# Performance work log

Measured on AMD Instinct MI355X. Metric: run time of the kernel, lower is better.

The kernel has to match this reference:

```python
import jax, jax.numpy as jnp
import numpy as np
import math

KV_STRIDE = 2
Q_STRIDE = 1
WAVE_LEN = 1000.0
POS_MAG = 1.0


def _pos_embed(h, w, h_kv, w_kv, q_stride, kv_stride, feat_dim):
    # Sinusoidal relative-position embeddings, matching get_position_embedding.
    h_idx = jnp.arange(h, dtype=jnp.float32) * q_stride
    w_idx = jnp.arange(w, dtype=jnp.float32) * q_stride
    h_kv_idx = jnp.arange(h_kv, dtype=jnp.float32) * kv_stride
    w_kv_idx = jnp.arange(w_kv, dtype=jnp.float32) * kv_stride
    h_diff = (h_idx[:, None] - h_kv_idx[None, :]) * POS_MAG  # (h, h_kv)
    w_diff = (w_idx[:, None] - w_kv_idx[None, :]) * POS_MAG  # (w, w_kv)
    feat_range = jnp.arange(feat_dim // 4, dtype=jnp.float32)
    dim_mat = WAVE_LEN ** (4.0 / feat_dim * feat_range)  # (feat_dim//4,)
    wd = w_diff[:, :, None] / dim_mat  # (w, w_kv, F)
    hd = h_diff[:, :, None] / dim_mat  # (h, h_kv, F)
    emb_x = jnp.concatenate([jnp.sin(wd), jnp.cos(wd)], axis=2)  # (w, w_kv, feat_dim//2)
    emb_y = jnp.concatenate([jnp.sin(hd), jnp.cos(hd)], axis=2)  # (h, h_kv, feat_dim//2)
    return emb_x, emb_y


def setup_inputs() -> dict:
    key = jax.random.key(0)
    ks = jax.random.split(key, 11)
    C = 288
    s = 1.0 / math.sqrt(C)
    return {
        'x_input': jax.random.normal(ks[0], (2, C, 64, 64), jnp.float32),
        'Wq': jax.random.normal(ks[1], (C, C), jnp.float32) * s,
        'Wk': jax.random.normal(ks[2], (C, C), jnp.float32) * s,
        'Wv': jax.random.normal(ks[3], (C, C), jnp.float32) * s,
        'Wx': jax.random.normal(ks[4], (C, C // 2), jnp.float32) * s,
        'Wy': jax.random.normal(ks[5], (C, C // 2), jnp.float32) * s,
        'Wproj': jax.random.normal(ks[6], (C, C), jnp.float32) * s,
        'bproj': jax.random.normal(ks[7], (C,), jnp.float32) * 0.02,
        'Wc': jax.random.normal(ks[8], (9, C), jnp.float32) * s,
        'bc': jax.random.normal(ks[9], (9,), jnp.float32) * 0.02,
        'gamma': jax.random.normal(ks[10], (1,), jnp.float32),
    }


def reference(x_input, Wq, Wk, Wv, Wx, Wy, Wproj, bproj, Wc, bc, gamma):
    M = Wc.shape[0]                       # num_mixtures
    n, C, h, w = x_input.shape
    d = Wq.shape[0] // M                  # qk_embed_dim (== v_dim)
    x_q = x_input                         # q_stride == 1
    x_kv = x_input[:, :, ::KV_STRIDE, ::KV_STRIDE]  # AvgPool2d(k=1, stride=2)
    h_kv, w_kv = x_kv.shape[2], x_kv.shape[3]

    # 1x1 convs as channel GEMMs
    q = jnp.einsum('nchw,oc->nohw', x_q, Wq).reshape(n, M, d, h * w)
    q = q.transpose(0, 1, 3, 2)                                    # (n,M,hw,d)
    k = jnp.einsum('nchw,oc->nohw', x_kv, Wk).reshape(n, M, d, h_kv * w_kv)

    emb_x, emb_y = _pos_embed(h, w, h_kv, w_kv, Q_STRIDE, KV_STRIDE, C)
    inv_sqrt2 = 1.0 / math.sqrt(2.0)
    pf_x = (emb_x @ Wx.T).reshape(w, w_kv, M, d).transpose(2, 0, 1, 3) * inv_sqrt2  # (M,w,w_kv,d)
    pf_y = (emb_y @ Wy.T).reshape(h, h_kv, M, d).transpose(2, 0, 1, 3) * inv_sqrt2  # (M,h,h_kv,d)

    energy = jnp.matmul(q, k).reshape(n, M, h, w, h_kv, w_kv)
    q5 = q.reshape(n, M, h, w, d)
    e_x = jnp.einsum('nmhwd,mwvd->nmhwv', q5, pf_x)  # (n,M,h,w,w_kv)
    e_y = jnp.einsum('nmhwd,mhud->nmhwu', q5, pf_y)  # (n,M,h,w,h_kv)
    energy = energy + e_x[:, :, :, :, None, :] + e_y[:, :, :, :, :, None]
    energy = energy.reshape(n, M, h * w, h_kv * w_kv)
    attn = jax.nn.softmax(energy, axis=3)

    # Learned per-mixture gating from mean query context
    context = q.transpose(0, 1, 3, 2).reshape(n, M * d, h * w).mean(axis=2)  # (n, M*d)
    mix_w = jax.nn.softmax(context @ Wc.T + bc, axis=1)                      # (n, M)
    attn = jnp.sum(attn * mix_w[:, :, None, None], axis=1)                   # (n,hw,hw_kv)

    v = jnp.einsum('nchw,oc->nohw', x_kv, Wv).reshape(n, M * d, h_kv * w_kv)
    v = v.transpose(0, 2, 1)                                                 # (n,hw_kv,M*d)
    out = jnp.matmul(attn, v).transpose(0, 2, 1).reshape(n, M * d, h, w)
    out = jnp.einsum('nchw,oc->nohw', out, Wproj) + bproj[None, :, None, None]
    return gamma[0] * out + x_input
```

## Files before the change

kernel.cpp:

```cpp
#include <hip/hip_runtime.h>
#include <math.h>

#define NB     2
#define CDIM   288
#define HW     4096
#define PKV    1024
#define MHEAD  9
#define DHEAD  32

typedef __attribute__((ext_vector_type(8))) short bf16x8;
typedef __attribute__((ext_vector_type(4))) float f32x4;

__device__ inline unsigned short f2bf(float x) {
    unsigned int u = __float_as_uint(x);
    u = (u + 0x7fffu + ((u >> 16) & 1u)) >> 16;
    return (unsigned short)u;
}


__global__ __launch_bounds__(256) void prep(const float* __restrict__ X,
        const float* __restrict__ Wq, const float* __restrict__ Wk,
        const float* __restrict__ Wv, const float* __restrict__ Wproj,
        const float* __restrict__ Wx, const float* __restrict__ Wy,
        unsigned short* __restrict__ XF, unsigned short* __restrict__ WFq,
        unsigned short* __restrict__ WFk, unsigned short* __restrict__ WFv,
        unsigned short* __restrict__ WFp, float* __restrict__ WTx,
        float* __restrict__ WTy, float* __restrict__ MX) {
    __shared__ float t32[32][133];
    __shared__ float t16[16][17];
    __shared__ float red[4];
    int b = blockIdx.x;
    int tid = threadIdx.x;
    if (b < 576) {
        int bx = b % 32, by = (b / 32) % 9, n = b / 288;
        int j0 = bx * 128, c0 = by * 32;
        int c = tid >> 3, f = tid & 7;
        const float* src = &X[((size_t)n * CDIM + c0 + c) * HW + j0];
#pragma unroll
        for (int l = 0; l < 4; ++l) {
            float4 v = *(const float4*)&src[(f + l * 8) * 4];
            *(float4*)&t32[c][(f + l * 8) * 4] = v;
        }
        __syncthreads();
        int cc = c0 >> 5;
#pragma unroll
        for (int l = 0; l < 4; ++l) {
            int g = l * 256 + tid;
            int s = g >> 7;
            int w = g & 127;
            int lane = w >> 1, e0 = (w & 1) * 4;
            int jl = s * 16 + (lane & 15);
            int cb = (lane >> 4) * 8 + e0;
            unsigned int w0 = f2bf(t32[cb + 0][jl]) | ((unsigned int)f2bf(t32[cb + 1][jl]) << 16);
            unsigned int w1 = f2bf(t32[cb + 2][jl]) | ((unsigned int)f2bf(t32[cb + 3][jl]) << 16);
            int jt = (j0 >> 4) + s;
            unsigned short* O = XF + (size_t)n * HW * CDIM + ((size_t)jt * 9 + cc) * 512 + lane * 8 + e0;
            uint2 pk = { w0, w1 };
            *(uint2*)O = pk;
        }
    } else if (b < 900) {
        int u = b - 576;
        int bx = u % 9, by = (u / 9) % 18, bz = u / 162;
        const float* W = bz ? Wy : Wx;
        float* WT      = bz ? WTy : WTx;
        int f0 = bx * 16, o0 = by * 16;
        int tx = tid & 15, ty = tid >> 4;
        t16[ty][tx] = W[(o0 + ty) * 144 + f0 + tx];
        __syncthreads();
        WT[(f0 + ty) * 288 + o0 + tx] = t16[tx][ty];
    } else if (b < 1062) {
        int t = b - 900;
        int sub = tid >> 6, lane = tid & 63;
        int ot = t / 9, cc = t % 9;
        const float* W = (sub == 0) ? Wq : (sub == 1) ? Wk : (sub == 2) ? Wv : Wproj;
        unsigned short* O = ((sub == 0) ? WFq : (sub == 1) ? WFk : (sub == 2) ? WFv : WFp)
                            + (size_t)t * 512;
        int o  = ot * 16 + (lane & 15);
        int c0 = cc * 32 + (lane >> 4) * 8;
        const float* src = W + (size_t)o * CDIM + c0;
        float4 f0 = *(const float4*)src, f1 = *(const float4*)(src + 4);
        unsigned int v0 = f2bf(f0.x) | ((unsigned int)f2bf(f0.y) << 16);
        unsigned int v1 = f2bf(f0.z) | ((unsigned int)f2bf(f0.w) << 16);
        unsigned int v2 = f2bf(f1.x) | ((unsigned int)f2bf(f1.y) << 16);
        unsigned int v3 = f2bf(f1.z) | ((unsigned int)f2bf(f1.w) << 16);
        uint4 pk = { v0, v1, v2, v3 };
        *(uint4*)(O + lane * 8) = pk;
    } else {
        int bid = b - 1062;
        const float* xr = X + (size_t)bid * HW;
        float s = 0.f;
        for (int j = tid; j < HW; j += 256) s += xr[j];
        for (int off = 32; off > 0; off >>= 1) s += __shfl_xor(s, off, 64);
        if ((tid & 63) == 0) red[tid >> 6] = s;
        __syncthreads();
        if (tid == 0) MX[bid] = (red[0] + red[1] + red[2] + red[3]) * (1.f / 4096.f);
    }
}

__global__ __launch_bounds__(256) void mid(
        const float* __restrict__ WTx, const float* __restrict__ WTy,
        unsigned short* __restrict__ FXb, unsigned short* __restrict__ FYb,
        const float* __restrict__ Wq, const float* __restrict__ MX,
        const float* __restrict__ Wc, const float* __restrict__ bc,
        float* __restrict__ MIXW,
        const unsigned short* __restrict__ WFq, const unsigned short* __restrict__ WFk,
        const unsigned short* __restrict__ WFv, const unsigned short* __restrict__ XF,
        unsigned short* __restrict__ Qf, unsigned short* __restrict__ KF,
        unsigned short* __restrict__ VF) {
    __shared__ float emb[144];
    __shared__ float ctx_s[NB * CDIM];
    __shared__ float lg[18];
    __shared__ __attribute__((aligned(16))) unsigned short tr[4][32][40];
    int b = blockIdx.x;
    int tid = threadIdx.x;

    if (b < 252) {
        int axis = b / 126;
        int dif  = b % 126;
        float diff = (float)(dif - 62);
        if (tid < 72) {
            float dm = expf(6.9077552789821368f * ((float)tid * (1.f / 72.f)));
            float t  = diff / dm;
            emb[tid]      = sinf(t);
            emb[72 + tid] = cosf(t);
        }
        __syncthreads();
        const float* WT = axis ? WTy : WTx;
        unsigned short* F = axis ? FYb : FXb;
        for (int o = tid; o < CDIM; o += 256) {
            float s = 0.f;
#pragma unroll 8
            for (int f = 0; f < 144; ++f) s += emb[f] * WT[f * 288 + o];
            int m = o >> 5, d = o & 31;
            F[(size_t)(m * 8 + (dif >> 4)) * 512 + ((dif & 15) + 16 * (d >> 3)) * 8 + (d & 7)]
                = f2bf(s * 0.70710678118654752f);
        }
    } else if (b == 252) {
        for (int idx = tid; idx < 1152; idx += 256) {
            int d = idx & 31, rr = (idx >> 5) & 1, mm = (idx >> 6) % 9, ax = idx / 576;
            int dif = 126 + rr;
            unsigned short* F = ax ? FYb : FXb;
            F[(size_t)(mm * 8 + 7) * 512 + ((dif & 15) + 16 * (d >> 3)) * 8 + (d & 7)] = 0;
        }
        for (int p = tid; p < NB * CDIM; p += 256) {
            int n = p / CDIM, o = p % CDIM;
            const float* wr = Wq + (size_t)o * CDIM;
            const float* mx = MX + n * CDIM;
            float s = 0.f;
            for (int c = 0; c < CDIM; c += 4) {
                float4 w4 = *(const float4*)&wr[c];
                float4 m4 = *(const float4*)&mx[c];
                s += w4.x * m4.x + w4.y * m4.y + w4.z * m4.z + w4.w * m4.w;
            }
            ctx_s[p] = s;
        }
        __syncthreads();
        if (tid < 18) {
            int n = tid / 9, j = tid % 9;
            float s = bc[j];
            for (int o = 0; o < CDIM; ++o) s += ctx_s[n * CDIM + o] * Wc[j * CDIM + o];
            lg[tid] = s;
        }
        __syncthreads();
        if (tid < 2) {
            float mx = -1e30f;
            for (int j = 0; j < 9; ++j) mx = fmaxf(mx, lg[tid * 9 + j]);
            float e[9], sm = 0.f;
            for (int j = 0; j < 9; ++j) { e[j] = __expf(lg[tid * 9 + j] - mx); sm += e[j]; }
            for (int j = 0; j < 9; ++j) MIXW[tid * 9 + j] = e[j] / sm;
        }
    } else {
        int bx = b - 253;
        int gx = bx % 40;
        int m  = (bx / 40) % 9;
        int n  = bx / 360;
        int wv = tid >> 6, lane = tid & 63;
        int lq = lane & 15, quad = lane >> 4;
        if (gx < 32) {
            int j0 = gx * 128;
            int jw = j0 + wv * 32;
            const unsigned short* Wb = WFq + ((size_t)(m * 2) * 9) * 512 + lane * 8;
            const unsigned short* Xb = XF + (size_t)n * HW * CDIM + ((size_t)(jw >> 4) * 9) * 512 + lane * 8;
            f32x4 acc[2][2] = {};
#pragma unroll
            for (int cc = 0; cc < 9; ++cc) {
                bf16x8 a0 = *(const bf16x8*)(Wb + (size_t)cc * 512);
                bf16x8 a1 = *(const bf16x8*)(Wb + (size_t)(9 + cc) * 512);
                bf16x8 b0 = *(const bf16x8*)(Xb + (size_t)cc * 512);
                bf16x8 b1 = *(const bf16x8*)(Xb + (size_t)(9 + cc) * 512);
                acc[0][0] = __builtin_amdgcn_mfma_f32_16x16x32_bf16(a0, b0, acc[0][0], 0, 0, 0);
                acc[0][1] = __builtin_amdgcn_mfma_f32_16x16x32_bf16(a0, b1, acc[0][1], 0, 0, 0);
                acc[1][0] = __builtin_amdgcn_mfma_f32_16x16x32_bf16(a1, b0, acc[1][0], 0, 0, 0);
                acc[1][1] = __builtin_amdgcn_mfma_f32_16x16x32_bf16(a1, b1, acc[1][1], 0, 0, 0);
            }
#pragma unroll
            for (int oi = 0; oi < 2; ++oi)
#pragma unroll
                for (int ji = 0; ji < 2; ++ji)
#pragma unroll
                    for (int r = 0; r < 4; ++r)
                        tr[wv][ji * 16 + lq][oi * 16 + quad * 4 + r] = f2bf(acc[oi][ji][r]);
            int jl = lane & 31, half = lane >> 5;
            bf16x8 v0 = *(const bf16x8*)&tr[wv][jl][half * 16];
            bf16x8 v1 = *(const bf16x8*)&tr[wv][jl][half * 16 + 8];
            unsigned short* Qm = Qf + ((size_t)(n * MHEAD + m) * HW + jw + jl) * 32 + half * 16;
            *(bf16x8*)Qm = v0;
            *(bf16x8*)(Qm + 8) = v1;
        } else {
            int p0 = (gx - 32) * 128;
            int pw = p0 + wv * 32;
            const unsigned short* XFn = XF + (size_t)n * HW * CDIM;
            size_t bidx[2];
#pragma unroll
            for (int pi = 0; pi < 2; ++pi) {
                int p   = pw + pi * 16 + lq;
                int pos = ((p >> 5) << 7) + ((p & 31) << 1);
                bidx[pi] = ((size_t)(pos >> 4) * 9) * 512 + ((pos & 15) + 16 * quad) * 8;
            }
            const unsigned short* Wkb = WFk + ((size_t)(m * 2) * 9) * 512 + lane * 8;
            const unsigned short* Wvb = WFv + ((size_t)(m * 2) * 9) * 512 + lane * 8;
            f32x4 ak[2][2] = {}, av[2][2] = {};
#pragma unroll
            for (int cc = 0; cc < 9; ++cc) {
                bf16x8 a0k = *(const bf16x8*)(Wkb + (size_t)cc * 512);
                bf16x8 a1k = *(const bf16x8*)(Wkb + (size_t)(9 + cc) * 512);
                bf16x8 a0v = *(const bf16x8*)(Wvb + (size_t)cc * 512);
                bf16x8 a1v = *(const bf16x8*)(Wvb + (size_t)(9 + cc) * 512);
                bf16x8 b0  = *(const bf16x8*)(XFn + bidx[0] + (size_t)cc * 512);
                bf16x8 b1  = *(const bf16x8*)(XFn + bidx[1] + (size_t)cc * 512);
                ak[0][0] = __builtin_amdgcn_mfma_f32_16x16x32_bf16(a0k, b0, ak[0][0], 0, 0, 0);
                ak[0][1] = __builtin_amdgcn_mfma_f32_16x16x32_bf16(a0k, b1, ak[0][1], 0, 0, 0);
                ak[1][0] = __builtin_amdgcn_mfma_f32_16x16x32_bf16(a1k, b0, ak[1][0], 0, 0, 0);
                ak[1][1] = __builtin_amdgcn_mfma_f32_16x16x32_bf16(a1k, b1, ak[1][1], 0, 0, 0);
                av[0][0] = __builtin_amdgcn_mfma_f32_16x16x32_bf16(a0v, b0, av[0][0], 0, 0, 0);
                av[0][1] = __builtin_amdgcn_mfma_f32_16x16x32_bf16(a0v, b1, av[0][1], 0, 0, 0);
                av[1][0] = __builtin_amdgcn_mfma_f32_16x16x32_bf16(a1v, b0, av[1][0], 0, 0, 0);
                av[1][1] = __builtin_amdgcn_mfma_f32_16x16x32_bf16(a1v, b1, av[1][1], 0, 0, 0);
            }
#pragma unroll
            for (int oi = 0; oi < 2; ++oi)
#pragma unroll
                for (int pi = 0; pi < 2; ++pi)
#pragma unroll
                    for (int r = 0; r < 4; ++r)
                        tr[wv][pi * 16 + lq][oi * 16 + quad * 4 + r] = f2bf(ak[oi][pi][r]);
            unsigned short* KFm = KF + (size_t)(n * MHEAD + m) * (PKV * 32);
#pragma unroll
            for (int pi = 0; pi < 2; ++pi) {
                bf16x8 v = *(const bf16x8*)&tr[wv][pi * 16 + lq][quad * 8];
                *(bf16x8*)(KFm + (size_t)((pw >> 4) + pi) * 512 + lane * 8) = v;
            }
#pragma unroll
            for (int oi = 0; oi < 2; ++oi)
#pragma unroll
                for (int pi = 0; pi < 2; ++pi)
#pragma unroll
                    for (int r = 0; r < 4; ++r)
                        tr[wv][oi * 16 + quad * 4 + r][pi * 16 + lq] = f2bf(av[oi][pi][r]);
            unsigned short* VFn = VF + (size_t)n * CDIM * PKV;
#pragma unroll
            for (int oi = 0; oi < 2; ++oi) {
                bf16x8 v = *(const bf16x8*)&tr[wv][oi * 16 + lq][quad * 8];
                *(bf16x8*)(VFn + (size_t)((m * 2 + oi) * 32 + (pw >> 5)) * 512 + lane * 8) = v;
            }
        }
    }
}

__global__ __launch_bounds__(512, 4) void attn_fused4(
        const unsigned short* __restrict__ Qf, const unsigned short* __restrict__ KF,
        const unsigned short* __restrict__ VF, const unsigned short* __restrict__ WFp,
        const unsigned short* __restrict__ FXb, const unsigned short* __restrict__ FYb,
        const float* __restrict__ MIXW, const float* __restrict__ bproj,
        const float* __restrict__ x, const float* __restrict__ gamma,
        float* __restrict__ OUT) {
    int n    = blockIdx.x >> 8;
    int i0   = (blockIdx.x & 255) * 16;
    int tid  = threadIdx.x;
    int wv   = tid >> 6;
    int lane = tid & 63;
    int lq   = lane & 15;
    int quad = lane >> 4;

    int bx_t = (i0 & 63) >> 4;
    int h    = i0 >> 6;
    int by_t = h >> 4;
    int dh   = h & 15;

    __shared__ __attribute__((aligned(16))) unsigned char RM[10752];
    float (*Rx_s)[82] = (float (*)[82])RM;
    float (*Ry_s)[82] = (float (*)[82])(RM + 5248);
    unsigned short (*Mt)[296] = (unsigned short (*)[296])RM;
    __shared__ __attribute__((aligned(16))) float ws_s[16][8];
    __shared__ __attribute__((aligned(16))) unsigned short tr[16][1032];

    float mixed[8][4];
#pragma unroll
    for (int t = 0; t < 8; ++t)
#pragma unroll
        for (int j = 0; j < 4; ++j) mixed[t][j] = 0.f;

    for (int m = 0; m < MHEAD; ++m) {
        const unsigned short* Qm  = Qf + ((size_t)(n * MHEAD + m) * HW + i0) * 32;
        const unsigned short* KmF = KF + (size_t)(n * MHEAD + m) * (PKV * 32);
        bf16x8 afrag = *(const bf16x8*)(Qm + (size_t)lq * 32 + quad * 8);

        if (wv < 5) {
            bf16x8 bR = *(const bf16x8*)(FXb + (size_t)(m * 8 + bx_t + wv) * 512 + lane * 8);
            f32x4 r = (f32x4){0.f, 0.f, 0.f, 0.f};
            r = __builtin_amdgcn_mfma_f32_16x16x32_bf16(afrag, bR, r, 0, 0, 0);
#pragma unroll
            for (int reg = 0; reg < 4; ++reg)
                Rx_s[quad * 4 + reg][wv * 16 + lq] = r[reg];
        } else {
            bf16x8 bR = *(const bf16x8*)(FYb + (size_t)(m * 8 + by_t + (wv - 5)) * 512 + lane * 8);
            f32x4 r = (f32x4){0.f, 0.f, 0.f, 0.f};
            r = __builtin_amdgcn_mfma_f32_16x16x32_bf16(afrag, bR, r, 0, 0, 0);
#pragma unroll
            for (int reg = 0; reg < 4; ++reg)
                Ry_s[quad * 4 + reg][(wv - 5) * 16 + lq] = r[reg];
        }
        if (wv < 2) {
            bf16x8 bR = *(const bf16x8*)(FYb + (size_t)(m * 8 + by_t + 3 + wv) * 512 + lane * 8);
            f32x4 r = (f32x4){0.f, 0.f, 0.f, 0.f};
            r = __builtin_amdgcn_mfma_f32_16x16x32_bf16(afrag, bR, r, 0, 0, 0);
#pragma unroll
            for (int reg = 0; reg < 4; ++reg)
                Ry_s[quad * 4 + reg][(3 + wv) * 16 + lq] = r[reg];
        }
        __syncthreads();

        bf16x8 kf[8];
#pragma unroll
        for (int t = 0; t < 8; ++t)
            kf[t] = *(const bf16x8*)(KmF + (size_t)(wv * 8 + t) * 512 + lane * 8);
        f32x4 acc[8];
#pragma unroll
        for (int t = 0; t < 8; ++t) acc[t] = (f32x4){0.f, 0.f, 0.f, 0.f};
#pragma unroll
        for (int t = 0; t < 8; ++t)
            acc[t] = __builtin_amdgcn_mfma_f32_16x16x32_bf16(afrag, kf[t], acc[t], 0, 0, 0);

        float exA[4], exB[4];
#pragma unroll
        for (int j = 0; j < 4; ++j) {
            int q = quad * 4 + j;
            exA[j] = Rx_s[q][q + 62 - 2 * lq];
            exB[j] = Rx_s[q][q + 30 - 2 * lq];
        }

        float rs[4] = {0.f, 0.f, 0.f, 0.f};
#pragma unroll
        for (int tp = 0; tp < 4; ++tp) {
            int u = wv * 4 + tp;
            float ey[4];
#pragma unroll
            for (int j = 0; j < 4; ++j) ey[j] = Ry_s[quad * 4 + j][dh + 62 - 2 * u];
#pragma unroll
            for (int half = 0; half < 2; ++half) {
                int t = tp * 2 + half;
#pragma unroll
                for (int j = 0; j < 4; ++j) {
                    float e = __expf(acc[t][j] + (half ? exB[j] : exA[j]) + ey[j]);
                    rs[j] += e;
                    acc[t][j] = e;
                }
            }
        }
#pragma unroll
        for (int j = 0; j < 4; ++j) {
            rs[j] += __shfl_xor(rs[j], 1, 64);
            rs[j] += __shfl_xor(rs[j], 2, 64);
            rs[j] += __shfl_xor(rs[j], 4, 64);
            rs[j] += __shfl_xor(rs[j], 8, 64);
        }
        if (lq == 0) {
#pragma unroll
            for (int j = 0; j < 4; ++j) ws_s[quad * 4 + j][wv] = rs[j];
        }
        __syncthreads();

        float wm = MIXW[n * MHEAD + m];
#pragma unroll
        for (int j = 0; j < 4; ++j) {
            int q = quad * 4 + j;
            float4 w0 = *(const float4*)&ws_s[q][0];
            float4 w1 = *(const float4*)&ws_s[q][4];
            float lt = (w0.x + w0.y) + (w0.z + w0.w) + (w1.x + w1.y) + (w1.z + w1.w);
            float fct = wm / lt;
#pragma unroll
            for (int t = 0; t < 8; ++t) mixed[t][j] += acc[t][j] * fct;
        }
    }

#pragma unroll
    for (int t = 0; t < 8; ++t)
#pragma unroll
        for (int j = 0; j < 4; ++j)
            tr[quad * 4 + j][wv * 128 + t * 16 + lq] = f2bf(mixed[t][j]);
    __syncthreads();

    const unsigned short* VFn = VF + (size_t)n * CDIM * PKV;
    f32x4 accpv[3];
#pragma unroll
    for (int idx = 0; idx < 3; ++idx) accpv[idx] = (f32x4){0.f, 0.f, 0.f, 0.f};
#pragma unroll 4
    for (int pc = 0; pc < 32; ++pc) {
        bf16x8 pf = *(const bf16x8*)&tr[lq][pc * 32 + quad * 8];
#pragma unroll
        for (int idx = 0; idx < 3; ++idx) {
            int ot = wv + idx * 8;
            if (ot < 18) {
                bf16x8 vf = *(const bf16x8*)(VFn + (size_t)(ot * 32 + pc) * 512 + lane * 8);
                accpv[idx] = __builtin_amdgcn_mfma_f32_16x16x32_bf16(pf, vf, accpv[idx], 0, 0, 0);
            }
        }
    }
#pragma unroll
    for (int idx = 0; idx < 3; ++idx) {
        int ot = wv + idx * 8;
        if (ot < 18) {
#pragma unroll
            for (int r = 0; r < 4; ++r)
                Mt[quad * 4 + r][ot * 16 + lq] = f2bf(accpv[idx][r]);
        }
    }
    __syncthreads();

    float g = gamma[0];
#pragma unroll
    for (int idx = 0; idx < 3; ++idx) {
        int ot = wv + idx * 8;
        if (ot >= 18) continue;
        f32x4 acc = (f32x4){0.f, 0.f, 0.f, 0.f};
#pragma unroll
        for (int cc = 0; cc < 9; ++cc) {
            bf16x8 af = *(const bf16x8*)(WFp + (size_t)(ot * 9 + cc) * 512 + lane * 8);
            bf16x8 bfm = *(const bf16x8*)&Mt[lq][cc * 32 + quad * 8];
            acc = __builtin_amdgcn_mfma_f32_16x16x32_bf16(af, bfm, acc, 0, 0, 0);
        }
#pragma unroll
        for (int r = 0; r < 4; ++r) {
            int o = ot * 16 + quad * 4 + r;
            size_t id = ((size_t)(n * CDIM) + o) * HW + i0 + lq;
            OUT[id] = g * (acc[r] + bproj[o]) + x[id];
        }
    }
}

extern "C" void kernel_launch(void* const* d_in, const int* in_sizes, int n_in,
                              void* d_out, int out_size, void* d_ws, size_t ws_size,
                              hipStream_t stream) {
    const float* x     = (const float*)d_in[0];
    const float* Wq    = (const float*)d_in[1];
    const float* Wk    = (const float*)d_in[2];
    const float* Wv    = (const float*)d_in[3];
    const float* Wx    = (const float*)d_in[4];
    const float* Wy    = (const float*)d_in[5];
    const float* Wproj = (const float*)d_in[6];
    const float* bproj = (const float*)d_in[7];
    const float* Wc    = (const float*)d_in[8];
    const float* bc    = (const float*)d_in[9];
    const float* gamma = (const float*)d_in[10];
    float* out = (float*)d_out;

    float* ws = (float*)d_ws;
    size_t off = 0;
    unsigned short* Qf  = (unsigned short*)(ws + off); off += (size_t)NB * MHEAD * HW * 32 / 2;
    unsigned short* KF  = (unsigned short*)(ws + off); off += (size_t)NB * MHEAD * PKV * 32 / 2;
    unsigned short* VF  = (unsigned short*)(ws + off); off += (size_t)NB * CDIM * PKV / 2;
    unsigned short* WFq = (unsigned short*)(ws + off); off += (size_t)CDIM * CDIM / 2;
    unsigned short* WFk = (unsigned short*)(ws + off); off += (size_t)CDIM * CDIM / 2;
    unsigned short* WFv = (unsigned short*)(ws + off); off += (size_t)CDIM * CDIM / 2;
    unsigned short* WFp = (unsigned short*)(ws + off); off += (size_t)CDIM * CDIM / 2;
    unsigned short* XF  = (unsigned short*)(ws + off); off += (size_t)NB * HW * CDIM / 2;
    float* WTx  = ws + off; off += 144 * 288;
    float* WTy  = ws + off; off += 144 * 288;
    unsigned short* FXb = (unsigned short*)(ws + off); off += (size_t)MHEAD * 8 * 512 / 2;
    unsigned short* FYb = (unsigned short*)(ws + off); off += (size_t)MHEAD * 8 * 512 / 2;
    float* MX   = ws + off; off += NB * CDIM;
    float* MIXW = ws + off; off += 32;

    prep<<<1638, 256, 0, stream>>>(x, Wq, Wk, Wv, Wproj, Wx, Wy,
                                   XF, WFq, WFk, WFv, WFp, WTx, WTy, MX);
    mid<<<973, 256, 0, stream>>>(WTx, WTy, FXb, FYb, Wq, MX, Wc, bc, MIXW,
                                 WFq, WFk, WFv, XF, Qf, KF, VF);
    attn_fused4<<<NB * HW / 16, 512, 0, stream>>>(Qf, KF, VF, WFp, FXb, FYb, MIXW,
                                                  bproj, x, gamma, out);
}
```

Measured before the change: 177.5 us.

## Precompute softmax denominators in a separate kernel to drop per-head block syncs

Adds a denom kernel that computes each head's row-sum of exponentials and stores the mixture weight divided by that sum per query row. The main attention kernel then reads these factors and accumulates the normalized exponentials directly. Each wave also computes its own Rx/Ry position-bias tiles into private shared memory, so the two __syncthreads per head disappear. In exchange, QK^T and the exponentials are computed twice, the per-wave bias work is redundant, and shared memory per block grows to about 58 KB, which may limit occupancy.

```diff
diff --git a/kernel.cpp b/kernel.cpp
--- a/kernel.cpp
+++ b/kernel.cpp
@@ -267,11 +267,114 @@
     }
 }
 
-__global__ __launch_bounds__(512, 4) void attn_fused4(
+__global__ __launch_bounds__(512, 4) void denom(
+        const unsigned short* __restrict__ Qf, const unsigned short* __restrict__ KF,
+        const unsigned short* __restrict__ FXb, const unsigned short* __restrict__ FYb,
+        const float* __restrict__ MIXW, float* __restrict__ FCT) {
+    int n  = blockIdx.z;
+    int m  = blockIdx.y;
+    int i0 = blockIdx.x * 16;
+    int tid  = threadIdx.x;
+    int wv   = tid >> 6;
+    int lane = tid & 63;
+    int lq   = lane & 15;
+    int quad = lane >> 4;
+    int bx_t = (i0 & 63) >> 4;
+    int h    = i0 >> 6;
+    int by_t = h >> 4;
+    int dh   = h & 15;
+
+    __shared__ float Rx_s[16][82];
+    __shared__ float Ry_s[16][82];
+    __shared__ float ws_s[16][8];
+
+    const unsigned short* Qm  = Qf + ((size_t)(n * MHEAD + m) * HW + i0) * 32;
+    const unsigned short* KmF = KF + (size_t)(n * MHEAD + m) * (PKV * 32);
+    bf16x8 afrag = *(const bf16x8*)(Qm + (size_t)lq * 32 + quad * 8);
+
+    if (wv < 5) {
+        bf16x8 bR = *(const bf16x8*)(FXb + (size_t)(m * 8 + bx_t + wv) * 512 + lane * 8);
+        f32x4 r = (f32x4){0.f, 0.f, 0.f, 0.f};
+        r = __builtin_amdgcn_mfma_f32_16x16x32_bf16(afrag, bR, r, 0, 0, 0);
+#pragma unroll
+        for (int reg = 0; reg < 4; ++reg)
+            Rx_s[quad * 4 + reg][wv * 16 + lq] = r[reg];
+    } else {
+        bf16x8 bR = *(const bf16x8*)(FYb + (size_t)(m * 8 + by_t + (wv - 5)) * 512 + lane * 8);
+        f32x4 r = (f32x4){0.f, 0.f, 0.f, 0.f};
+        r = __builtin_amdgcn_mfma_f32_16x16x32_bf16(afrag, bR, r, 0, 0, 0);
+#pragma unroll
+        for (int reg = 0; reg < 4; ++reg)
+            Ry_s[quad * 4 + reg][(wv - 5) * 16 + lq] = r[reg];
+    }
+    if (wv < 2) {
+        bf16x8 bR = *(const bf16x8*)(FYb + (size_t)(m * 8 + by_t + 3 + wv) * 512 + lane * 8);
+        f32x4 r = (f32x4){0.f, 0.f, 0.f, 0.f};
+        r = __builtin_amdgcn_mfma_f32_16x16x32_bf16(afrag, bR, r, 0, 0, 0);
+#pragma unroll
+        for (int reg = 0; reg < 4; ++reg)
+            Ry_s[quad * 4 + reg][(3 + wv) * 16 + lq] = r[reg];
+    }
+    __syncthreads();
+
+    bf16x8 kf[8];
+#pragma unroll
+    for (int t = 0; t < 8; ++t)
+        kf[t] = *(const bf16x8*)(KmF + (size_t)(wv * 8 + t) * 512 + lane * 8);
+    f32x4 acc[8];
+#pragma unroll
+    for (int t = 0; t < 8; ++t) acc[t] = (f32x4){0.f, 0.f, 0.f, 0.f};
+#pragma unroll
+    for (int t = 0; t < 8; ++t)
+        acc[t] = __builtin_amdgcn_mfma_f32_16x16x32_bf16(afrag, kf[t], acc[t], 0, 0, 0);
+
+    float exA[4], exB[4];
+#pragma unroll
+    for (int j = 0; j < 4; ++j) {
+        int q = quad * 4 + j;
+        exA[j] = Rx_s[q][q + 62 - 2 * lq];
+        exB[j] = Rx_s[q][q + 30 - 2 * lq];
+    }
+    float rs[4] = {0.f, 0.f, 0.f, 0.f};
+#pragma unroll
+    for (int tp = 0; tp < 4; ++tp) {
+        int u = wv * 4 + tp;
+        float ey[4];
+#pragma unroll
+        for (int j = 0; j < 4; ++j) ey[j] = Ry_s[quad * 4 + j][dh + 62 - 2 * u];
+#pragma unroll
+        for (int half = 0; half < 2; ++half) {
+            int t = tp * 2 + half;
+#pragma unroll
+            for (int j = 0; j < 4; ++j)
+                rs[j] += __expf(acc[t][j] + (half ? exB[j] : exA[j]) + ey[j]);
+        }
+    }
+#pragma unroll
+    for (int j = 0; j < 4; ++j) {
+        rs[j] += __shfl_xor(rs[j], 1, 64);
+        rs[j] += __shfl_xor(rs[j], 2, 64);
+        rs[j] += __shfl_xor(rs[j], 4, 64);
+        rs[j] += __shfl_xor(rs[j], 8, 64);
+    }
+    if (lq == 0) {
+#pragma unroll
+        for (int j = 0; j < 4; ++j) ws_s[quad * 4 + j][wv] = rs[j];
+    }
+    __syncthreads();
+    if (tid < 16) {
+        float4 w0 = *(const float4*)&ws_s[tid][0];
+        float4 w1 = *(const float4*)&ws_s[tid][4];
+        float lt = (w0.x + w0.y) + (w0.z + w0.w) + (w1.x + w1.y) + (w1.z + w1.w);
+        FCT[(size_t)(n * MHEAD + m) * HW + i0 + tid] = MIXW[n * MHEAD + m] / lt;
+    }
+}
+
+__global__ __launch_bounds__(512, 4) void attn_fused5(
         const unsigned short* __restrict__ Qf, const unsigned short* __restrict__ KF,
         const unsigned short* __restrict__ VF, const unsigned short* __restrict__ WFp,
         const unsigned short* __restrict__ FXb, const unsigned short* __restrict__ FYb,
-        const float* __restrict__ MIXW, const float* __restrict__ bproj,
+        const float* __restrict__ FCT, const float* __restrict__ bproj,
         const float* __restrict__ x, const float* __restrict__ gamma,
         float* __restrict__ OUT) {
     int n    = blockIdx.x >> 8;
@@ -286,13 +389,13 @@
     int h    = i0 >> 6;
     int by_t = h >> 4;
     int dh   = h & 15;
-
-    __shared__ __attribute__((aligned(16))) unsigned char RM[10752];
-    float (*Rx_s)[82] = (float (*)[82])RM;
-    float (*Ry_s)[82] = (float (*)[82])(RM + 5248);
-    unsigned short (*Mt)[296] = (unsigned short (*)[296])RM;
-    __shared__ __attribute__((aligned(16))) float ws_s[16][8];
-    __shared__ __attribute__((aligned(16))) unsigned short tr[16][1032];
+    int ty0  = (dh + 56 - 8 * wv) >> 4;
+
+    __shared__ __attribute__((aligned(16))) unsigned char RM[58368];
+    float* RxW = (float*)(RM + wv * 7296);
+    float* RyW = (float*)(RM + wv * 7296 + 5184);
+    unsigned short (*tr)[1032] = (unsigned short (*)[1032])RM;
+    unsigned short (*Mt)[296]  = (unsigned short (*)[296])(RM + 33024);
 
     float mixed[8][4];
 #pragma unroll
@@ -305,30 +408,29 @@
         const unsigned short* KmF = KF + (size_t)(n * MHEAD + m) * (PKV * 32);
         bf16x8 afrag = *(const bf16x8*)(Qm + (size_t)lq * 32 + quad * 8);
 
-        if (wv < 5) {
-            bf16x8 bR = *(const bf16x8*)(FXb + (size_t)(m * 8 + bx_t + wv) * 512 + lane * 8);
+        float fct[4];
+#pragma unroll
+        for (int j = 0; j < 4; ++j)
+            fct[j] = FCT[(size_t)(n * MHEAD + m) * HW + i0 + quad * 4 + j];
+
+#pragma unroll
+        for (int t = 0; t < 5; ++t) {
+            bf16x8 bR = *(const bf16x8*)(FXb + (size_t)(m * 8 + bx_t + t) * 512 + lane * 8);
             f32x4 r = (f32x4){0.f, 0.f, 0.f, 0.f};
             r = __builtin_amdgcn_mfma_f32_16x16x32_bf16(afrag, bR, r, 0, 0, 0);
 #pragma unroll
             for (int reg = 0; reg < 4; ++reg)
-                Rx_s[quad * 4 + reg][wv * 16 + lq] = r[reg];
-        } else {
-            bf16x8 bR = *(const bf16x8*)(FYb + (size_t)(m * 8 + by_t + (wv - 5)) * 512 + lane * 8);
+                RxW[(quad * 4 + reg) * 81 + t * 16 + lq] = r[reg];
+        }
+#pragma unroll
+        for (int t = 0; t < 2; ++t) {
+            bf16x8 bR = *(const bf16x8*)(FYb + (size_t)(m * 8 + by_t + ty0 + t) * 512 + lane * 8);
             f32x4 r = (f32x4){0.f, 0.f, 0.f, 0.f};
             r = __builtin_amdgcn_mfma_f32_16x16x32_bf16(afrag, bR, r, 0, 0, 0);
 #pragma unroll
             for (int reg = 0; reg < 4; ++reg)
-                Ry_s[quad * 4 + reg][(wv - 5) * 16 + lq] = r[reg];
-        }
-        if (wv < 2) {
-            bf16x8 bR = *(const bf16x8*)(FYb + (size_t)(m * 8 + by_t + 3 + wv) * 512 + lane * 8);
-            f32x4 r = (f32x4){0.f, 0.f, 0.f, 0.f};
-            r = __builtin_amdgcn_mfma_f32_16x16x32_bf16(afrag, bR, r, 0, 0, 0);
-#pragma unroll
-            for (int reg = 0; reg < 4; ++reg)
-                Ry_s[quad * 4 + reg][(3 + wv) * 16 + lq] = r[reg];
-        }
-        __syncthreads();
+                RyW[(quad * 4 + reg) * 33 + t * 16 + lq] = r[reg];
+        }
 
         bf16x8 kf[8];
 #pragma unroll
@@ -345,53 +447,26 @@
 #pragma unroll
         for (int j = 0; j < 4; ++j) {
             int q = quad * 4 + j;
-            exA[j] = Rx_s[q][q + 62 - 2 * lq];
-            exB[j] = Rx_s[q][q + 30 - 2 * lq];
-        }
-
-        float rs[4] = {0.f, 0.f, 0.f, 0.f};
+            exA[j] = RxW[q * 81 + q + 62 - 2 * lq];
+            exB[j] = RxW[q * 81 + q + 30 - 2 * lq];
+        }
 #pragma unroll
         for (int tp = 0; tp < 4; ++tp) {
             int u = wv * 4 + tp;
+            int yc = dh + 62 - 2 * u - ty0 * 16;
             float ey[4];
 #pragma unroll
-            for (int j = 0; j < 4; ++j) ey[j] = Ry_s[quad * 4 + j][dh + 62 - 2 * u];
+            for (int j = 0; j < 4; ++j) ey[j] = RyW[(quad * 4 + j) * 33 + yc];
 #pragma unroll
             for (int half = 0; half < 2; ++half) {
                 int t = tp * 2 + half;
 #pragma unroll
-                for (int j = 0; j < 4; ++j) {
-                    float e = __expf(acc[t][j] + (half ? exB[j] : exA[j]) + ey[j]);
-                    rs[j] += e;
-                    acc[t][j] = e;
-                }
-            }
-        }
-#pragma unroll
-        for (int j = 0; j < 4; ++j) {
-            rs[j] += __shfl_xor(rs[j], 1, 64);
-            rs[j] += __shfl_xor(rs[j], 2, 64);
-            rs[j] += __shfl_xor(rs[j], 4, 64);
-            rs[j] += __shfl_xor(rs[j], 8, 64);
-        }
-        if (lq == 0) {
-#pragma unroll
-            for (int j = 0; j < 4; ++j) ws_s[quad * 4 + j][wv] = rs[j];
-        }
-        __syncthreads();
-
-        float wm = MIXW[n * MHEAD + m];
-#pragma unroll
-        for (int j = 0; j < 4; ++j) {
-            int q = quad * 4 + j;
-            float4 w0 = *(const float4*)&ws_s[q][0];
-            float4 w1 = *(const float4*)&ws_s[q][4];
-            float lt = (w0.x + w0.y) + (w0.z + w0.w) + (w1.x + w1.y) + (w1.z + w1.w);
-            float fct = wm / lt;
-#pragma unroll
-            for (int t = 0; t < 8; ++t) mixed[t][j] += acc[t][j] * fct;
-        }
-    }
+                for (int j = 0; j < 4; ++j)
+                    mixed[t][j] += __expf(acc[t][j] + (half ? exB[j] : exA[j]) + ey[j]) * fct[j];
+            }
+        }
+    }
+    __syncthreads();
 
 #pragma unroll
     for (int t = 0; t < 8; ++t)
@@ -480,11 +555,13 @@
     unsigned short* FYb = (unsigned short*)(ws + off); off += (size_t)MHEAD * 8 * 512 / 2;
     float* MX   = ws + off; off += NB * CDIM;
     float* MIXW = ws + off; off += 32;
+    float* FCT  = ws + off; off += (size_t)NB * MHEAD * HW;
 
     prep<<<1638, 256, 0, stream>>>(x, Wq, Wk, Wv, Wproj, Wx, Wy,
                                    XF, WFq, WFk, WFv, WFp, WTx, WTy, MX);
     mid<<<973, 256, 0, stream>>>(WTx, WTy, FXb, FYb, Wq, MX, Wc, bc, MIXW,
                                  WFq, WFk, WFv, XF, Qf, KF, VF);
-    attn_fused4<<<NB * HW / 16, 512, 0, stream>>>(Qf, KF, VF, WFp, FXb, FYb, MIXW,
+    denom<<<dim3(256, MHEAD, NB), 512, 0, stream>>>(Qf, KF, FXb, FYb, MIXW, FCT);
+    attn_fused5<<<NB * HW / 16, 512, 0, stream>>>(Qf, KF, VF, WFp, FXb, FYb, FCT,
                                                   bproj, x, gamma, out);
 }
```

After: 193.9 us. +9.2%, slower.
